# Kernel tuning notes

Hardware: AMD Instinct MI355X
Metric: run time of the kernel (lower is better)

## Reference

```python
import jax, jax.numpy as jnp
import numpy as np

C, H, R, INTER = 1024, 16, 16, 2816  # hidden, heads, lora rank, mlp intermediate
B, N = 2, 2048
EPS = 1e-5


def setup_inputs() -> dict:
    key = jax.random.key(0)
    ks = iter(jax.random.split(key, 48))
    w = lambda shape: jax.random.normal(next(ks), shape, jnp.float32) * 0.02
    d = {}
    d["x"] = jax.random.normal(next(ks), (B, N, C), jnp.float32)
    d["y"] = jax.random.normal(next(ks), (B, N, C), jnp.float32)
    d["c"] = jax.random.normal(next(ks), (B, C), jnp.float32)
    # LayerNorms
    d["gx_w"] = jnp.ones((C,)); d["gx_b"] = jnp.zeros((C,))
    d["gy_w"] = jnp.ones((C,)); d["gy_b"] = jnp.zeros((C,))
    # adaLN: SiLU -> Linear(C, 6C)
    d["ada_w"] = w((C, 6 * C)); d["ada_b"] = jnp.zeros((6 * C,))
    # two DoRA cross-attentions
    for p in ("xy", "yx"):
        d[p + "_qkv"] = w((C, 3 * C))
        d[p + "_mag"] = jnp.ones((1, H, 1, 1))
        d[p + "_la"] = w((C, R))
        d[p + "_lb"] = w((R, C))
        d[p + "_proj"] = w((C, C))
    # two HGRN recurrent attentions
    for p in ("ax", "ay"):
        d[p + "_wi"] = w((C, C))
        d[p + "_wf"] = w((C, C))
        d[p + "_wg"] = w((C, C))
        d[p + "_wo"] = w((C, C))
        d[p + "_gn"] = jnp.ones((C,))
    # two gated MLPs
    for p in ("mx", "my"):
        d[p + "_gate"] = w((C, 2 * INTER))
        d[p + "_down"] = w((INTER, C))
    return d


def _ln(v, wgt, b):
    m = v.mean(-1, keepdims=True)
    var = ((v - m) ** 2).mean(-1, keepdims=True)
    return (v - m) / jnp.sqrt(var + EPS) * wgt + b


def _modulate(v, shift, scale):
    return v * (1.0 + scale[:, None, :]) + shift[:, None, :]


def _dora_attn(q_in, Wqkv, mag, la, lb, Wp):
    # NOTE: source ignores key/value args -> self-attention on query stream
    Bq, Nq, Cq = q_in.shape
    D = Cq // H
    qkv = (q_in @ Wqkv).reshape(Bq, Nq, 3, H, D).transpose(2, 0, 3, 1, 4)
    q, k, v = qkv[0], qkv[1], qkv[2]  # [B,H,N,D]
    delta = (q_in @ la) @ lb  # LoRA delta injected into Q
    q = q + mag * delta.reshape(Bq, Nq, H, D).transpose(0, 2, 1, 3)
    attn = jax.nn.softmax(jnp.einsum('bhnd,bhmd->bhnm', q, k) * (D ** -0.5), axis=-1)
    o = jnp.einsum('bhnm,bhmd->bhnd', attn, v).transpose(0, 2, 1, 3).reshape(Bq, Nq, Cq)
    return o @ Wp


def _hgrn_attn(v, wi, wf, wg, wo, gn):
    Bv, Nv, Cv = v.shape
    D = Cv // H
    f = jax.nn.sigmoid(v @ wf)
    i = jax.nn.silu(v @ wi) * (1.0 - f)
    def step(h, ft_it):
        ft, it = ft_it
        h = ft * h + it
        return h, h
    _, hs = jax.lax.scan(step, jnp.zeros((Bv, Cv), v.dtype),
                         (f.transpose(1, 0, 2), i.transpose(1, 0, 2)))
    h = hs.transpose(1, 0, 2).reshape(Bv, Nv, H, D)
    h = h / jnp.sqrt((h * h).mean(-1, keepdims=True) + EPS)  # per-head RMSNorm
    h = (h * gn.reshape(H, D)).reshape(Bv, Nv, Cv)
    return (h * jax.nn.silu(v @ wg)) @ wo


def _mlp(v, wgate, wdown):
    u = v @ wgate
    gate, val = jnp.split(u, 2, axis=-1)
    return (jax.nn.silu(gate) * val) @ wdown


def reference(x, y, c, gx_w, gx_b, gy_w, gy_b, ada_w, ada_b,
              xy_qkv, xy_mag, xy_la, xy_lb, xy_proj,
              yx_qkv, yx_mag, yx_la, yx_lb, yx_proj,
              ax_wi, ax_wf, ax_wg, ax_wo, ax_gn,
              ay_wi, ay_wf, ay_wg, ay_wo, ay_gn,
              mx_gate, mx_down, my_gate, my_down):
    mods = jax.nn.silu(c) @ ada_w + ada_b
    sh_msa, sc_msa, g_msa, sh_mlp, sc_mlp, g_mlp = jnp.split(mods, 6, axis=1)
    x_norm = _ln(x, gx_w, gx_b)
    y_norm = _ln(y, gy_w, gy_b)
    x = x + g_msa[:, None, :] * _dora_attn(x_norm, xy_qkv, xy_mag, xy_la, xy_lb, xy_proj)
    y = y + g_msa[:, None, :] * _dora_attn(y_norm, yx_qkv, yx_mag, yx_la, yx_lb, yx_proj)
    x = x + g_msa[:, None, :] * _hgrn_attn(_modulate(x_norm, sh_msa, sc_msa), ax_wi, ax_wf, ax_wg, ax_wo, ax_gn)
    y = y + g_msa[:, None, :] * _hgrn_attn(_modulate(y_norm, sh_msa, sc_msa), ay_wi, ay_wf, ay_wg, ay_wo, ay_gn)
    x = x + g_mlp[:, None, :] * _mlp(_modulate(_ln(x, gx_w, gx_b), sh_mlp, sc_mlp), mx_gate, mx_down)
    y = y + g_mlp[:, None, :] * _mlp(_modulate(_ln(y, gy_w, gy_b), sh_mlp, sc_mlp), my_gate, my_down)
    return (x, y)
```

## Files before the change

kernel.cpp:

```cpp
#include <hip/hip_runtime.h>
#include <stdint.h>

#define NTOK 2048
#define CDIM 1024
#define ROWS 4096
#define MODS_STRIDE 6144
#define INTERDIM 2816
#define NCHUNK 32
#define CHLEN (NTOK/NCHUNK)

typedef unsigned short u16;
typedef __bf16 bf16x8 __attribute__((ext_vector_type(8)));
typedef float f32x4 __attribute__((ext_vector_type(4)));
typedef u16 u16x8 __attribute__((ext_vector_type(8)));

__device__ __forceinline__ float b2f(u16 u){
  union { unsigned int i; float f; } v; v.i = ((unsigned int)u) << 16; return v.f;
}
__device__ __forceinline__ u16 f2b(float f){
  union { float f; unsigned int i; } v; v.f = f;
  unsigned int i = v.i;
  unsigned int r = i + 0x7FFFu + ((i >> 16) & 1u);
  return (u16)(r >> 16);
}
__device__ __forceinline__ float sigm(float x){ return 1.f/(1.f+__expf(-x)); }
__device__ __forceinline__ float wredsum(float v){
#pragma unroll
  for (int o=32;o>0;o>>=1) v += __shfl_xor(v,o);
  return v;
}
__device__ __forceinline__ void async16(const void* g, void* l){
  __builtin_amdgcn_global_load_lds(
      (const __attribute__((address_space(1))) unsigned int*)g,
      (__attribute__((address_space(3))) unsigned int*)l, 16, 0, 0);
}

__global__ __launch_bounds__(512) void gemm_bt(
    const u16* __restrict__ Ain, const u16* __restrict__ Bt,
    int M, int N, int K, int epi,
    u16* __restrict__ outB,
    float* __restrict__ dest, const float* __restrict__ gate)
{
  __shared__ u16 smem[2][2][2][8192];

  const int nwg  = gridDim.x * gridDim.y;
  const int orig = blockIdx.y * gridDim.x + blockIdx.x;
  const int qch  = nwg >> 3, rch = nwg & 7;
  const int xcd  = orig & 7, loc = orig >> 3;
  const int swzb = (xcd < rch ? xcd*(qch+1) : rch*(qch+1) + (xcd-rch)*qch) + loc;
  const int m0 = (swzb / gridDim.x) * 256;
  const int n0 = (swzb % gridDim.x) * 256;

  const int kchunk = K / gridDim.z;
  const int kbase  = blockIdx.z * kchunk;
  const int NT = kchunk >> 6;

  const int tid = threadIdx.x;
  const int w = tid >> 6, lane = tid & 63;
  const int quad = lane >> 4, l16 = lane & 15;
  const int wm = w >> 2, wn = w & 3;
  const int sx = (l16 & 7) << 4;

  int soff[2];
#pragma unroll
  for (int j=0;j<2;++j){
    const int row = (w*2 + j)*8 + (lane >> 3);
    soff[j] = row*(K*2) + (((lane & 7) ^ (row & 7)) << 4);
  }

  const char* pA0 = (const char*)(Ain + (size_t)m0*K       + kbase);
  const char* pA1 = (const char*)(Ain + (size_t)(m0+128)*K + kbase);
  const char* pB0 = (const char*)(Bt  + (size_t)n0*K       + kbase);
  const char* pB1 = (const char*)(Bt  + (size_t)(n0+128)*K + kbase);

  auto stage = [&](const char* base, int t, u16* region){
#pragma unroll
    for (int j=0;j<2;++j)
      async16(base + (size_t)t*128 + soff[j], (char*)region + (w*2+j)*1024);
  };

  f32x4 acc[8][4] = {};
  bf16x8 af[4][2];
  bf16x8 bq[4][2];

  stage(pA0, 0, &smem[0][0][0][0]);
  stage(pA1, 0, &smem[0][0][1][0]);
  stage(pB0, 0, &smem[0][1][0][0]);
  stage(pB1, 0, &smem[0][1][1][0]);
  if (NT > 1){
    stage(pA0, 1, &smem[1][0][0][0]);
    asm volatile("s_waitcnt vmcnt(2)" ::: "memory");
  } else {
    asm volatile("s_waitcnt vmcnt(0)" ::: "memory");
  }
  __builtin_amdgcn_s_barrier();

#pragma unroll 1
  for (int t=0; t<NT; ++t){
    const int s  = t & 1;
    const int s1 = s ^ 1;
    const char* Ah = (const char*)&smem[s][0][wm][0];
    const char* Bh = (const char*)&smem[s][1][wn>>1][0];
    const int bb = (wn & 1) * 64;

#pragma unroll
    for (int mf=0; mf<4; ++mf)
#pragma unroll
      for (int ks=0; ks<2; ++ks){
        const int b = ((mf*16 + l16)*128 + ks*64 + quad*16) ^ sx;
        af[mf][ks] = *reinterpret_cast<const bf16x8*>(Ah + b);
      }
#pragma unroll
    for (int nf=0; nf<2; ++nf)
#pragma unroll
      for (int ks=0; ks<2; ++ks){
        const int b = ((bb + nf*16 + l16)*128 + ks*64 + quad*16) ^ sx;
        bq[nf][ks] = *reinterpret_cast<const bf16x8*>(Bh + b);
      }
    if (t+1 < NT) stage(pA1, t+1, &smem[s1][0][1][0]);
    __builtin_amdgcn_sched_barrier(0);
    __builtin_amdgcn_s_barrier();
    asm volatile("s_waitcnt lgkmcnt(0)" ::: "memory");
    __builtin_amdgcn_sched_barrier(0);
    __builtin_amdgcn_s_setprio(1);
#pragma unroll
    for (int mf=0; mf<4; ++mf)
#pragma unroll
      for (int nf=0; nf<2; ++nf)
#pragma unroll
        for (int ks=0; ks<2; ++ks)
          acc[mf][nf] = __builtin_amdgcn_mfma_f32_16x16x32_bf16(af[mf][ks], bq[nf][ks], acc[mf][nf], 0,0,0);
    __builtin_amdgcn_s_setprio(0);
    __builtin_amdgcn_sched_barrier(0);
    __builtin_amdgcn_s_barrier();

#pragma unroll
    for (int nf=0; nf<2; ++nf)
#pragma unroll
      for (int ks=0; ks<2; ++ks){
        const int b = ((bb + (2+nf)*16 + l16)*128 + ks*64 + quad*16) ^ sx;
        bq[2+nf][ks] = *reinterpret_cast<const bf16x8*>(Bh + b);
      }
    if (t+1 < NT) stage(pB0, t+1, &smem[s1][1][0][0]);
    __builtin_amdgcn_sched_barrier(0);
    __builtin_amdgcn_s_barrier();
    asm volatile("s_waitcnt lgkmcnt(0)" ::: "memory");
    __builtin_amdgcn_sched_barrier(0);
    __builtin_amdgcn_s_setprio(1);
#pragma unroll
    for (int mf=0; mf<4; ++mf)
#pragma unroll
      for (int nf=0; nf<2; ++nf)
#pragma unroll
        for (int ks=0; ks<2; ++ks)
          acc[mf][2+nf] = __builtin_amdgcn_mfma_f32_16x16x32_bf16(af[mf][ks], bq[2+nf][ks], acc[mf][2+nf], 0,0,0);
    __builtin_amdgcn_s_setprio(0);
    __builtin_amdgcn_sched_barrier(0);
    __builtin_amdgcn_s_barrier();

#pragma unroll
    for (int mf=0; mf<4; ++mf)
#pragma unroll
      for (int ks=0; ks<2; ++ks){
        const int b = ((64 + mf*16 + l16)*128 + ks*64 + quad*16) ^ sx;
        af[mf][ks] = *reinterpret_cast<const bf16x8*>(Ah + b);
      }
    if (t+1 < NT) stage(pB1, t+1, &smem[s1][1][1][0]);
    __builtin_amdgcn_sched_barrier(0);
    __builtin_amdgcn_s_barrier();
    asm volatile("s_waitcnt lgkmcnt(0)" ::: "memory");
    __builtin_amdgcn_sched_barrier(0);
    __builtin_amdgcn_s_setprio(1);
#pragma unroll
    for (int mf=0; mf<4; ++mf)
#pragma unroll
      for (int nf=0; nf<2; ++nf)
#pragma unroll
        for (int ks=0; ks<2; ++ks)
          acc[4+mf][2+nf] = __builtin_amdgcn_mfma_f32_16x16x32_bf16(af[mf][ks], bq[2+nf][ks], acc[4+mf][2+nf], 0,0,0);
    __builtin_amdgcn_s_setprio(0);
    __builtin_amdgcn_sched_barrier(0);
    __builtin_amdgcn_s_barrier();

    if (t+2 < NT) stage(pA0, t+2, &smem[s][0][0][0]);
    __builtin_amdgcn_sched_barrier(0);
    __builtin_amdgcn_s_barrier();
    __builtin_amdgcn_s_setprio(1);
#pragma unroll
    for (int mf=0; mf<4; ++mf)
#pragma unroll
      for (int nf=0; nf<2; ++nf)
#pragma unroll
        for (int ks=0; ks<2; ++ks)
          acc[4+mf][nf] = __builtin_amdgcn_mfma_f32_16x16x32_bf16(af[mf][ks], bq[nf][ks], acc[4+mf][nf], 0,0,0);
    __builtin_amdgcn_s_setprio(0);
    __builtin_amdgcn_sched_barrier(0);
    if (t+2 < NT) asm volatile("s_waitcnt vmcnt(2)" ::: "memory");
    else          asm volatile("s_waitcnt vmcnt(0)" ::: "memory");
    __builtin_amdgcn_s_barrier();
  }

#pragma unroll
  for (int i=0;i<8;++i){
    const int row = m0 + wm*128 + (i>>2)*64 + (i&3)*16 + quad*4;
#pragma unroll
    for (int j=0;j<4;++j){
      const int col = n0 + wn*64 + j*16 + l16;
#pragma unroll
      for (int r=0;r<4;++r){
        const float v = acc[i][j][r];
        const size_t idx = (size_t)(row + r)*N + col;
        if (epi==1){ outB[idx] = f2b(v); }
        else {
          const int b = (row + r) >> 11;
          atomicAdd(&dest[idx], gate[b*MODS_STRIDE + col] * v);
        }
      }
    }
  }
}

struct TDesc { const float* src; u16* dst; int rows; int cols; int base; int dstride; int doff; };
struct TPack { TDesc d[16]; };

__global__ __launch_bounds__(256) void transpose_all(TPack p, int nmat)
{
  __shared__ float t[32][33];
  const int bid = blockIdx.x;
  int mi = 0;
#pragma unroll 1
  while (mi+1 < nmat && bid >= p.d[mi+1].base) ++mi;
  const TDesc D = p.d[mi];
  const int tid2   = bid - D.base;
  const int tilesx = D.cols >> 5;
  const int r0 = (tid2 / tilesx) * 32;
  const int c0 = (tid2 % tilesx) * 32;
  const int tx = threadIdx.x & 31, ty = threadIdx.x >> 5;
  for (int i=ty;i<32;i+=8)
    t[i][tx] = D.src[(size_t)(r0+i)*D.cols + c0 + tx];
  __syncthreads();
  for (int i=ty;i<32;i+=8)
    D.dst[(size_t)(c0+i)*D.dstride + D.doff + r0 + tx] = f2b(t[tx][i]);
}

__global__ __launch_bounds__(256) void lora_fold(
    const float* __restrict__ la, const float* __restrict__ lb,
    const float* __restrict__ mag, u16* __restrict__ WqkvT)
{
  const unsigned idx = blockIdx.x*256u + threadIdx.x;
  const int k = idx & 1023, n = idx >> 10;
  float s = 0.f;
#pragma unroll
  for (int r=0;r<16;++r)
    s = fmaf(la[k*16+r], lb[r*1024+n], s);
  const float m = mag[n>>6];
  const unsigned o = (unsigned)n*1024u + k;
  WqkvT[o] = f2b(b2f(WqkvT[o]) + m*s);
}

__global__ __launch_bounds__(256) void ln_kernel(
    const float* __restrict__ xin,
    const float* __restrict__ w, const float* __restrict__ bias,
    const float* __restrict__ mods, int sh_off, int sc_off,
    u16* __restrict__ out_norm, u16* __restrict__ out_mod,
    float* __restrict__ out_xw)
{
  const int row = blockIdx.x;
  const int b = row >> 11;
  const int t = threadIdx.x;
  float v[4];
#pragma unroll
  for (int e=0;e<4;++e)
    v[e] = xin[(size_t)row*CDIM + t*4+e];
  float s  = v[0]+v[1]+v[2]+v[3];
  float ss = v[0]*v[0]+v[1]*v[1]+v[2]*v[2]+v[3]*v[3];
  s = wredsum(s); ss = wredsum(ss);
  __shared__ float rs[4], rss[4];
  const int wv = t>>6;
  if ((t&63)==0){ rs[wv]=s; rss[wv]=ss; }
  __syncthreads();
  s  = rs[0]+rs[1]+rs[2]+rs[3];
  ss = rss[0]+rss[1]+rss[2]+rss[3];
  const float mean = s * (1.f/1024.f);
  const float var  = ss * (1.f/1024.f) - mean*mean;
  const float rinv = rsqrtf(var + 1e-5f);
#pragma unroll
  for (int e=0;e<4;++e){
    const int c = t*4+e;
    const float nv = (v[e]-mean)*rinv*w[c] + bias[c];
    if (out_norm) out_norm[(size_t)row*CDIM+c] = f2b(nv);
    if (out_mod){
      const float sc = mods[b*MODS_STRIDE + sc_off + c];
      const float sh = mods[b*MODS_STRIDE + sh_off + c];
      out_mod[(size_t)row*CDIM+c] = f2b(nv*(1.f+sc)+sh);
    }
    if (out_xw) out_xw[(size_t)row*CDIM+c] = v[e];
  }
}

__global__ __launch_bounds__(256) void ada_init(
    const float* __restrict__ ab, float* __restrict__ mods)
{
  const int j = blockIdx.x*256 + threadIdx.x;
  const int jj = (j >= MODS_STRIDE) ? j - MODS_STRIDE : j;
  mods[j] = ab[jj];
}

__global__ __launch_bounds__(256) void ada_split(
    const float* __restrict__ cin, const float* __restrict__ aw,
    float* __restrict__ mods)
{
  const int j  = blockIdx.x*256 + threadIdx.x;
  const int k0 = blockIdx.y*64;
  float s0 = 0.f, s1 = 0.f;
  for (int k=k0; k<k0+64; ++k){
    const float wv = aw[(size_t)k*MODS_STRIDE + j];
    const float c0 = cin[k], c1 = cin[CDIM + k];
    s0 = fmaf(c0*sigm(c0), wv, s0);
    s1 = fmaf(c1*sigm(c1), wv, s1);
  }
  atomicAdd(&mods[j], s0);
  atomicAdd(&mods[MODS_STRIDE + j], s1);
}

__global__ __launch_bounds__(256) void attn_mfma(
    const u16* __restrict__ qkv, u16* __restrict__ AH)
{
  __shared__ u16 Kl[64*64];
  __shared__ u16 Vt[64*64];
  __shared__ u16 Pl[4][16*64];
  const int t = threadIdx.x;
  const int w = t>>6, lane = t&63;
  const int l16 = lane&15, quad = lane>>4;
  const int qt = blockIdx.x, h = blockIdx.y, b = blockIdx.z;
  const size_t rowbase = (size_t)b*NTOK;

  bf16x8 qf[2];
  {
    const size_t gr = rowbase + qt*64 + w*16 + l16;
    const u16* qp = qkv + gr*3072 + h*64;
#pragma unroll
    for (int kw=0; kw<2; ++kw){
      const u16x8 qa = *reinterpret_cast<const u16x8*>(qp + kw*32 + quad*8);
#pragma unroll
      for (int j=0;j<8;++j)
        qf[kw][j] = (__bf16)(b2f(qa[j]) * 0.125f);
    }
  }

  const u16* ksrc[2]; int kwr[2];
#pragma unroll
  for (int it=0; it<2; ++it){
    const int e = it*256 + t;
    const int key = e>>3, ch = e&7;
    ksrc[it] = qkv + (rowbase + key)*3072 + 1024 + h*64 + ch*8;
    kwr[it]  = key*128 + ((ch ^ (key&7)) << 4);
  }
  const u16* vsrc[2]; int vwr[2][8];
#pragma unroll
  for (int it=0; it<2; ++it){
    const int d0 = (w*2 + it)*8;
    vsrc[it] = qkv + (rowbase + lane)*3072 + 2048 + h*64 + d0;
#pragma unroll
    for (int j=0;j<8;++j){
      const int d = d0 + j;
      vwr[it][j] = d*128 + (((lane>>3) ^ (d&7)) << 4) + (lane&7)*2;
    }
  }
  int ra[4][2], pr[2], pw[4][2];
#pragma unroll
  for (int x=0; x<4; ++x)
#pragma unroll
    for (int kw=0; kw<2; ++kw)
      ra[x][kw] = (x*16 + l16)*128 + (((kw*4 + quad) ^ (l16&7)) << 4);
#pragma unroll
  for (int kw=0; kw<2; ++kw)
    pr[kw] = l16*128 + (((kw*4 + quad) ^ (l16&7)) << 4);
#pragma unroll
  for (int mt=0; mt<4; ++mt)
#pragma unroll
    for (int rp=0; rp<2; ++rp){
      const int bo = (mt*16 + quad*4 + rp*2)*2;
      pw[mt][rp] = l16*128 + (((bo>>4) ^ (l16&7)) << 4) + (bo & 15);
    }

  const size_t KSTRIDE = (size_t)64*3072;

  u16x8 kA[2], vA[2], kB[2], vB[2];
#pragma unroll
  for (int it=0; it<2; ++it){
    kA[it] = *reinterpret_cast<const u16x8*>(ksrc[it]);
    vA[it] = *reinterpret_cast<const u16x8*>(vsrc[it]);
  }

  float l_part = 0.f;
  f32x4 oacc[4] = {};
  char* const pb = (char*)&Pl[w][0];

  auto step = [&](u16x8 (&kk)[2], u16x8 (&vv)[2], int kbn,
                  u16x8 (&kn)[2], u16x8 (&vn)[2]){
#pragma unroll
    for (int it=0; it<2; ++it){
      *reinterpret_cast<u16x8*>((char*)Kl + kwr[it]) = kk[it];
#pragma unroll
      for (int j=0;j<8;++j)
        *reinterpret_cast<u16*>((char*)Vt + vwr[it][j]) = vv[it][j];
    }
    __syncthreads();
    {
      const size_t off = (size_t)kbn * KSTRIDE;
#pragma unroll
      for (int it=0; it<2; ++it){
        kn[it] = *reinterpret_cast<const u16x8*>(ksrc[it] + off);
        vn[it] = *reinterpret_cast<const u16x8*>(vsrc[it] + off);
      }
    }
    f32x4 sacc[4] = {};
#pragma unroll
    for (int kw=0; kw<2; ++kw)
#pragma unroll
      for (int mt=0; mt<4; ++mt){
        const bf16x8 af = *reinterpret_cast<const bf16x8*>((char*)Kl + ra[mt][kw]);
        sacc[mt] = __builtin_amdgcn_mfma_f32_16x16x32_bf16(af, qf[kw], sacc[mt], 0,0,0);
      }
#pragma unroll
    for (int mt=0; mt<4; ++mt)
#pragma unroll
      for (int r=0;r<4;++r){
        const float pv = __expf(sacc[mt][r]);
        sacc[mt][r] = pv;
        l_part += pv;
      }
#pragma unroll
    for (int mt=0; mt<4; ++mt)
#pragma unroll
      for (int rp=0; rp<2; ++rp){
        const unsigned hi = __float_as_uint(sacc[mt][rp*2+1]);
        const unsigned lo = __float_as_uint(sacc[mt][rp*2]);
        *reinterpret_cast<unsigned*>(pb + pw[mt][rp]) = (hi & 0xFFFF0000u) | (lo >> 16);
      }
#pragma unroll
    for (int kw=0; kw<2; ++kw){
      const bf16x8 pa = *reinterpret_cast<const bf16x8*>(pb + pr[kw]);
#pragma unroll
      for (int dt=0; dt<4; ++dt){
        const bf16x8 vb = *reinterpret_cast<const bf16x8*>((char*)Vt + ra[dt][kw]);
        oacc[dt] = __builtin_amdgcn_mfma_f32_16x16x32_bf16(pa, vb, oacc[dt], 0,0,0);
      }
    }
    __syncthreads();
  };

#pragma unroll 1
  for (int kb=0; kb<32; kb+=2){
    step(kA, vA, (kb+1 < 32 ? kb+1 : 31), kB, vB);
    step(kB, vB, (kb+2 < 32 ? kb+2 : 31), kA, vA);
  }

  float l_run = l_part;
  l_run += __shfl_xor(l_run, 16);
  l_run += __shfl_xor(l_run, 32);

  float li4[4];
#pragma unroll
  for (int r=0;r<4;++r) li4[r] = __shfl(l_run, quad*4+r);
#pragma unroll
  for (int r=0;r<4;++r){
    const size_t grow = rowbase + qt*64 + w*16 + quad*4 + r;
#pragma unroll
    for (int dt=0; dt<4; ++dt)
      AH[grow*2048 + h*64 + dt*16 + l16] = f2b(oacc[dt][r] / li4[r]);
  }
}

__global__ __launch_bounds__(256) void scan_p1(
    const u16* __restrict__ FIG, float* __restrict__ cA, float* __restrict__ cH)
{
  const unsigned int idx = blockIdx.x*256u + threadIdx.x;
  const unsigned int c = idx & 1023u, chunk = (idx>>10)&(NCHUNK-1), b = idx>>15;
  float A = 1.f, h = 0.f;
  const size_t base = ((size_t)b*NTOK + chunk*CHLEN) * 3072;
  for (int t=0;t<CHLEN;++t){
    const float F = b2f(FIG[base + (size_t)t*3072 + c]);
    const float I = b2f(FIG[base + (size_t)t*3072 + 1024 + c]);
    const float f = sigm(F);
    const float il = I*sigm(I) * (1.f - f);
    A *= f;
    h = fmaf(f, h, il);
  }
  cA[idx] = A; cH[idx] = h;
}

__global__ __launch_bounds__(256) void scan_p2(
    const float* __restrict__ cA, const float* __restrict__ cH, float* __restrict__ Hinit)
{
  const unsigned int idx = blockIdx.x*256u + threadIdx.x;
  const unsigned int b = idx>>10, c = idx&1023u;
  float h = 0.f;
#pragma unroll
  for (int ch=0;ch<NCHUNK;++ch){
    const unsigned int q = (b*NCHUNK + ch)*1024 + c;
    Hinit[q] = h;
    h = fmaf(cA[q], h, cH[q]);
  }
}

__global__ __launch_bounds__(256) void scan_p3(
    const u16* __restrict__ FIG, const float* __restrict__ Hinit, u16* __restrict__ Hb)
{
  const unsigned int idx = blockIdx.x*256u + threadIdx.x;
  const unsigned int c = idx & 1023u, chunk = (idx>>10)&(NCHUNK-1), b = idx>>15;
  float h = Hinit[idx];
  const size_t base = ((size_t)b*NTOK + chunk*CHLEN) * 3072;
  const size_t obase = ((size_t)b*NTOK + chunk*CHLEN) * CDIM;
  for (int t=0;t<CHLEN;++t){
    const float F = b2f(FIG[base + (size_t)t*3072 + c]);
    const float I = b2f(FIG[base + (size_t)t*3072 + 1024 + c]);
    const float f = sigm(F);
    const float il = I*sigm(I) * (1.f - f);
    h = fmaf(f, h, il);
    Hb[obase + (size_t)t*CDIM + c] = f2b(h);
  }
}

__global__ __launch_bounds__(256) void hgrn_post(
    const u16* __restrict__ Hb, const u16* __restrict__ FIG,
    const float* __restrict__ gn, u16* __restrict__ AH)
{
  const int row = blockIdx.x;
  const int t = threadIdx.x;
  float hv[4]; float ss = 0.f;
#pragma unroll
  for (int e=0;e<4;++e){
    hv[e] = b2f(Hb[(size_t)row*CDIM + t*4 + e]);
    ss = fmaf(hv[e], hv[e], ss);
  }
#pragma unroll
  for (int o=1;o<16;o<<=1) ss += __shfl_xor(ss, o);
  const float rinv = rsqrtf(ss*(1.f/64.f) + 1e-5f);
#pragma unroll
  for (int e=0;e<4;++e){
    const int c = t*4+e;
    const float g = b2f(FIG[(size_t)row*3072 + 2048 + c]);
    AH[(size_t)row*2048 + 1024 + c] = f2b(hv[e]*rinv*gn[c] * g*sigm(g));
  }
}

__global__ __launch_bounds__(256) void act_kernel(
    const u16* __restrict__ U, u16* __restrict__ A)
{
  const unsigned int i = blockIdx.x*256u + threadIdx.x;
  const unsigned int r = i / INTERDIM, j = i % INTERDIM;
  const float g = b2f(U[(size_t)r*(2*INTERDIM) + j]);
  const float v = b2f(U[(size_t)r*(2*INTERDIM) + INTERDIM + j]);
  A[i] = f2b(g*sigm(g)*v);
}

__global__ __launch_bounds__(256) void store_out(
    const float* __restrict__ xw, float* __restrict__ out)
{
  const unsigned int i = blockIdx.x*256u + threadIdx.x;
  out[i] = xw[i];
}

__global__ __launch_bounds__(256) void fill_fail(float* __restrict__ out)
{
  const unsigned int i = blockIdx.x*256u + threadIdx.x;
  out[i] = 1234.5f;
}

static void run_stream(hipStream_t stream,
    const float* Xin, const float* LNW, const float* LNB,
    const float* MAG, const float* LA, const float* LBw, const float* GN,
    float* mods, float* xw, float* outp,
    u16* WqkvT, const u16* WpwT, const u16* WhgrnT,
    const u16* WgateT, const u16* WdownT,
    u16* x_norm, u16* v_h, u16* qkvb, u16* delta, u16* AH,
    float* cA, float* cH, float* Hinit, u16* U, u16* actb)
{
  u16* FIG    = qkvb;
  u16* Hb     = delta;
  u16* mlp_in = x_norm;

  lora_fold<<<4096,256,0,stream>>>(LA, LBw, MAG, WqkvT);

  ln_kernel<<<ROWS,256,0,stream>>>(Xin, LNW, LNB, mods, 0, 1024, x_norm, v_h, xw);

  gemm_bt<<<dim3(12,16),512,0,stream>>>(x_norm, WqkvT, ROWS,3072,1024, 1, qkvb, nullptr, nullptr);
  attn_mfma<<<dim3(32,16,2),256,0,stream>>>(qkvb, AH);

  gemm_bt<<<dim3(12,16),512,0,stream>>>(v_h, WhgrnT, ROWS,3072,1024, 1, FIG, nullptr, nullptr);
  scan_p1<<<2*NCHUNK*1024/256,256,0,stream>>>(FIG, cA, cH);
  scan_p2<<<8,256,0,stream>>>(cA, cH, Hinit);
  scan_p3<<<2*NCHUNK*1024/256,256,0,stream>>>(FIG, Hinit, Hb);
  hgrn_post<<<ROWS,256,0,stream>>>(Hb, FIG, GN, AH);

  gemm_bt<<<dim3(4,16,4),512,0,stream>>>(AH, WpwT, ROWS,1024,2048, 2, nullptr, xw, mods+2048);

  ln_kernel<<<ROWS,256,0,stream>>>(xw, LNW, LNB, mods, 3072, 4096, nullptr, mlp_in, nullptr);
  gemm_bt<<<dim3(22,16),512,0,stream>>>(mlp_in, WgateT, ROWS,5632,1024, 1, U, nullptr, nullptr);
  act_kernel<<<ROWS*INTERDIM/256,256,0,stream>>>(U, actb);
  gemm_bt<<<dim3(4,16,4),512,0,stream>>>(actb, WdownT, ROWS,1024,2816, 2, nullptr, xw, mods+5120);

  store_out<<<ROWS*CDIM/256,256,0,stream>>>(xw, outp);
}

extern "C" void kernel_launch(void* const* d_in, const int* in_sizes, int n_in,
                              void* d_out, int out_size, void* d_ws, size_t ws_size,
                              hipStream_t stream)
{
  const float* X    = (const float*)d_in[0];
  const float* Y    = (const float*)d_in[1];
  const float* Cc   = (const float*)d_in[2];
  const float* GXW  = (const float*)d_in[3];
  const float* GXB  = (const float*)d_in[4];
  const float* GYW  = (const float*)d_in[5];
  const float* GYB  = (const float*)d_in[6];
  const float* ADAW = (const float*)d_in[7];
  const float* ADAB = (const float*)d_in[8];
  const float* XY_QKV = (const float*)d_in[9];
  const float* XY_MAG = (const float*)d_in[10];
  const float* XY_LA  = (const float*)d_in[11];
  const float* XY_LB  = (const float*)d_in[12];
  const float* XY_PROJ= (const float*)d_in[13];
  const float* YX_QKV = (const float*)d_in[14];
  const float* YX_MAG = (const float*)d_in[15];
  const float* YX_LA  = (const float*)d_in[16];
  const float* YX_LB  = (const float*)d_in[17];
  const float* YX_PROJ= (const float*)d_in[18];
  const float* AX_WI = (const float*)d_in[19];
  const float* AX_WF = (const float*)d_in[20];
  const float* AX_WG = (const float*)d_in[21];
  const float* AX_WO = (const float*)d_in[22];
  const float* AX_GN = (const float*)d_in[23];
  const float* AY_WI = (const float*)d_in[24];
  const float* AY_WF = (const float*)d_in[25];
  const float* AY_WG = (const float*)d_in[26];
  const float* AY_WO = (const float*)d_in[27];
  const float* AY_GN = (const float*)d_in[28];
  const float* MX_GATE = (const float*)d_in[29];
  const float* MX_DOWN = (const float*)d_in[30];
  const float* MY_GATE = (const float*)d_in[31];
  const float* MY_DOWN = (const float*)d_in[32];
  float* OUT = (float*)d_out;

  char* p = (char*)d_ws;
  size_t off = 0;
  auto alloc = [&](size_t bytes)->char*{
    char* r = p + off;
    off = (off + bytes + 255) & ~(size_t)255;
    return r;
  };
  float* mods  = (float*)alloc(2*MODS_STRIDE*sizeof(float));
  float* xw_x  = (float*)alloc((size_t)ROWS*CDIM*sizeof(float));
  float* xw_y  = (float*)alloc((size_t)ROWS*CDIM*sizeof(float));
  u16* WqkvT0  = (u16*)alloc((size_t)3072*1024*2);
  u16* WqkvT1  = (u16*)alloc((size_t)3072*1024*2);
  u16* WpwT0   = (u16*)alloc((size_t)1024*2048*2);
  u16* WpwT1   = (u16*)alloc((size_t)1024*2048*2);
  u16* WhgrnT0 = (u16*)alloc((size_t)3072*1024*2);
  u16* WhgrnT1 = (u16*)alloc((size_t)3072*1024*2);
  u16* WgateT0 = (u16*)alloc((size_t)5632*1024*2);
  u16* WgateT1 = (u16*)alloc((size_t)5632*1024*2);
  u16* WdownT0 = (u16*)alloc((size_t)1024*2816*2);
  u16* WdownT1 = (u16*)alloc((size_t)1024*2816*2);
  u16* x_norm  = (u16*)alloc((size_t)ROWS*CDIM*2);
  u16* v_h     = (u16*)alloc((size_t)ROWS*CDIM*2);
  u16* qkvb    = (u16*)alloc((size_t)ROWS*3072*2);
  u16* delta   = (u16*)alloc((size_t)ROWS*CDIM*2);
  u16* AH      = (u16*)alloc((size_t)ROWS*2048*2);
  float* cA    = (float*)alloc((size_t)2*NCHUNK*1024*sizeof(float));
  float* cH    = (float*)alloc((size_t)2*NCHUNK*1024*sizeof(float));
  float* Hinit = (float*)alloc((size_t)2*NCHUNK*1024*sizeof(float));
  u16* U       = (u16*)alloc((size_t)ROWS*5632*2);
  u16* actb    = (u16*)alloc((size_t)ROWS*INTERDIM*2);

  if (off > ws_size){
    fill_fail<<<(2*ROWS*CDIM)/256,256,0,stream>>>(OUT);
    return;
  }

  ada_init<<<2*MODS_STRIDE/256,256,0,stream>>>(ADAB, mods);
  ada_split<<<dim3(MODS_STRIDE/256,16),256,0,stream>>>(Cc, ADAW, mods);

  TPack tp; int base = 0; int ndesc = 0;
  auto add = [&](const float* s, u16* d2, int rows, int cols, int dstride, int doff){
    tp.d[ndesc].src = s; tp.d[ndesc].dst = d2;
    tp.d[ndesc].rows = rows; tp.d[ndesc].cols = cols; tp.d[ndesc].base = base;
    tp.d[ndesc].dstride = dstride; tp.d[ndesc].doff = doff;
    base += (rows>>5)*(cols>>5); ++ndesc;
  };
  add(XY_QKV,  WqkvT0, 1024, 3072, 1024, 0);
  add(XY_PROJ, WpwT0,  1024, 1024, 2048, 0);
  add(AX_WO,   WpwT0,  1024, 1024, 2048, 1024);
  add(AX_WF, WhgrnT0,               1024, 1024, 1024, 0);
  add(AX_WI, WhgrnT0 + 1024*1024,   1024, 1024, 1024, 0);
  add(AX_WG, WhgrnT0 + 2*1024*1024, 1024, 1024, 1024, 0);
  add(MX_GATE, WgateT0, 1024, 5632, 1024, 0);
  add(MX_DOWN, WdownT0, 2816, 1024, 2816, 0);
  add(YX_QKV,  WqkvT1, 1024, 3072, 1024, 0);
  add(YX_PROJ, WpwT1,  1024, 1024, 2048, 0);
  add(AY_WO,   WpwT1,  1024, 1024, 2048, 1024);
  add(AY_WF, WhgrnT1,               1024, 1024, 1024, 0);
  add(AY_WI, WhgrnT1 + 1024*1024,   1024, 1024, 1024, 0);
  add(AY_WG, WhgrnT1 + 2*1024*1024, 1024, 1024, 1024, 0);
  add(MY_GATE, WgateT1, 1024, 5632, 1024, 0);
  add(MY_DOWN, WdownT1, 2816, 1024, 2816, 0);
  transpose_all<<<base,256,0,stream>>>(tp, ndesc);

  run_stream(stream, X, GXW, GXB, XY_MAG, XY_LA, XY_LB, AX_GN,
             mods, xw_x, OUT,
             WqkvT0, WpwT0, WhgrnT0, WgateT0, WdownT0,
             x_norm, v_h, qkvb, delta, AH,
             cA, cH, Hinit, U, actb);

  run_stream(stream, Y, GYW, GYB, YX_MAG, YX_LA, YX_LB, AY_GN,
             mods, xw_y, OUT + (size_t)ROWS*CDIM,
             WqkvT1, WpwT1, WhgrnT1, WgateT1, WdownT1,
             x_norm, v_h, qkvb, delta, AH,
             cA, cH, Hinit, U, actb);
}
```

Before: 1.262 ms.

## Fuse SiLU-gating into gate GEMM epilogue and move attention to 32x32 MFMA

The MLP gate weight columns are interleaved during transpose so gate and value columns sit next to each other. The gate GEMM epilogue can then compute silu(g)*v with a lane shuffle and write the activation directly, which drops the separate act kernel and the U intermediate buffer. Separately, the attention kernel is rewritten to use 32x32x16 MFMAs over 128-query tiles. Probabilities are kept in registers through packed bf16 converts and permlane32 swaps instead of round-tripping through LDS. This adds register pressure and halves the attention grid size.

```diff
diff --git a/kernel.cpp b/kernel.cpp
--- a/kernel.cpp
+++ b/kernel.cpp
@@ -12,7 +12,9 @@
 typedef unsigned short u16;
 typedef __bf16 bf16x8 __attribute__((ext_vector_type(8)));
 typedef float f32x4 __attribute__((ext_vector_type(4)));
+typedef float f32x16 __attribute__((ext_vector_type(16)));
 typedef u16 u16x8 __attribute__((ext_vector_type(8)));
+typedef unsigned int u32x4 __attribute__((ext_vector_type(4)));
 
 __device__ __forceinline__ float b2f(u16 u){
   union { unsigned int i; float f; } v; v.i = ((unsigned int)u) << 16; return v.f;
@@ -33,6 +35,14 @@
   __builtin_amdgcn_global_load_lds(
       (const __attribute__((address_space(1))) unsigned int*)g,
       (__attribute__((address_space(3))) unsigned int*)l, 16, 0, 0);
+}
+__device__ __forceinline__ unsigned cvt_pk_bf16(float lo, float hi){
+  unsigned r;
+  asm("v_cvt_pk_bf16_f32 %0, %1, %2" : "=v"(r) : "v"(lo), "v"(hi));
+  return r;
+}
+__device__ __forceinline__ void permlane32_swap(unsigned &a, unsigned &b){
+  asm volatile("v_permlane32_swap_b32 %0, %1" : "+v"(a), "+v"(b));
 }
 
 __global__ __launch_bounds__(512) void gemm_bt(
@@ -211,7 +221,13 @@
         const float v = acc[i][j][r];
         const size_t idx = (size_t)(row + r)*N + col;
         if (epi==1){ outB[idx] = f2b(v); }
-        else {
+        else if (epi==3){
+          const float pv2 = __shfl_xor(v, 1);
+          if ((l16 & 1) == 0){
+            const float o = v*sigm(v)*pv2;
+            outB[(size_t)(row + r)*(N>>1) + (col>>1)] = f2b(o);
+          }
+        } else {
           const int b = (row + r) >> 11;
           atomicAdd(&dest[idx], gate[b*MODS_STRIDE + col] * v);
         }
@@ -220,7 +236,7 @@
   }
 }
 
-struct TDesc { const float* src; u16* dst; int rows; int cols; int base; int dstride; int doff; };
+struct TDesc { const float* src; u16* dst; int rows; int cols; int base; int dstride; int doff; int ileave; };
 struct TPack { TDesc d[16]; };
 
 __global__ __launch_bounds__(256) void transpose_all(TPack p, int nmat)
@@ -239,8 +255,11 @@
   for (int i=ty;i<32;i+=8)
     t[i][tx] = D.src[(size_t)(r0+i)*D.cols + c0 + tx];
   __syncthreads();
-  for (int i=ty;i<32;i+=8)
-    D.dst[(size_t)(c0+i)*D.dstride + D.doff + r0 + tx] = f2b(t[tx][i]);
+  for (int i=ty;i<32;i+=8){
+    int n = c0 + i;
+    if (D.ileave) n = (n < D.ileave) ? 2*n : 2*(n - D.ileave) + 1;
+    D.dst[(size_t)n*D.dstride + D.doff + r0 + tx] = f2b(t[tx][i]);
+  }
 }
 
 __global__ __launch_bounds__(256) void lora_fold(
@@ -328,23 +347,22 @@
 {
   __shared__ u16 Kl[64*64];
   __shared__ u16 Vt[64*64];
-  __shared__ u16 Pl[4][16*64];
   const int t = threadIdx.x;
   const int w = t>>6, lane = t&63;
-  const int l16 = lane&15, quad = lane>>4;
+  const int l32 = lane & 31, hi = lane >> 5;
   const int qt = blockIdx.x, h = blockIdx.y, b = blockIdx.z;
   const size_t rowbase = (size_t)b*NTOK;
 
-  bf16x8 qf[2];
+  bf16x8 qf[4];
   {
-    const size_t gr = rowbase + qt*64 + w*16 + l16;
+    const size_t gr = rowbase + qt*128 + w*32 + l32;
     const u16* qp = qkv + gr*3072 + h*64;
 #pragma unroll
-    for (int kw=0; kw<2; ++kw){
-      const u16x8 qa = *reinterpret_cast<const u16x8*>(qp + kw*32 + quad*8);
+    for (int ds=0; ds<4; ++ds){
+      const u16x8 qa = *reinterpret_cast<const u16x8*>(qp + ds*16 + hi*8);
 #pragma unroll
       for (int j=0;j<8;++j)
-        qf[kw][j] = (__bf16)(b2f(qa[j]) * 0.125f);
+        qf[ds][j] = (__bf16)(b2f(qa[j]) * 0.125f);
     }
   }
 
@@ -367,22 +385,24 @@
       vwr[it][j] = d*128 + (((lane>>3) ^ (d&7)) << 4) + (lane&7)*2;
     }
   }
-  int ra[4][2], pr[2], pw[4][2];
-#pragma unroll
-  for (int x=0; x<4; ++x)
-#pragma unroll
-    for (int kw=0; kw<2; ++kw)
-      ra[x][kw] = (x*16 + l16)*128 + (((kw*4 + quad) ^ (l16&7)) << 4);
-#pragma unroll
-  for (int kw=0; kw<2; ++kw)
-    pr[kw] = l16*128 + (((kw*4 + quad) ^ (l16&7)) << 4);
-#pragma unroll
-  for (int mt=0; mt<4; ++mt)
-#pragma unroll
-    for (int rp=0; rp<2; ++rp){
-      const int bo = (mt*16 + quad*4 + rp*2)*2;
-      pw[mt][rp] = l16*128 + (((bo>>4) ^ (l16&7)) << 4) + (bo & 15);
+  int kra[2][4];
+#pragma unroll
+  for (int st=0; st<2; ++st)
+#pragma unroll
+    for (int ds=0; ds<4; ++ds){
+      const int key = st*32 + l32;
+      kra[st][ds] = key*128 + (((ds*2 + hi) ^ (key&7)) << 4);
     }
+  int vra[2][2][2];
+#pragma unroll
+  for (int st=0; st<2; ++st)
+#pragma unroll
+    for (int ks=0; ks<2; ++ks)
+#pragma unroll
+      for (int dt=0; dt<2; ++dt){
+        const int d = dt*32 + l32;
+        vra[st][ks][dt] = d*128 + (((st*4 + ks*2 + hi) ^ (d&7)) << 4);
+      }
 
   const size_t KSTRIDE = (size_t)64*3072;
 
@@ -394,8 +414,7 @@
   }
 
   float l_part = 0.f;
-  f32x4 oacc[4] = {};
-  char* const pb = (char*)&Pl[w][0];
+  f32x16 oacc[2] = {};
 
   auto step = [&](u16x8 (&kk)[2], u16x8 (&vv)[2], int kbn,
                   u16x8 (&kn)[2], u16x8 (&vn)[2]){
@@ -415,37 +434,43 @@
         vn[it] = *reinterpret_cast<const u16x8*>(vsrc[it] + off);
       }
     }
-    f32x4 sacc[4] = {};
-#pragma unroll
-    for (int kw=0; kw<2; ++kw)
-#pragma unroll
-      for (int mt=0; mt<4; ++mt){
-        const bf16x8 af = *reinterpret_cast<const bf16x8*>((char*)Kl + ra[mt][kw]);
-        sacc[mt] = __builtin_amdgcn_mfma_f32_16x16x32_bf16(af, qf[kw], sacc[mt], 0,0,0);
-      }
-#pragma unroll
-    for (int mt=0; mt<4; ++mt)
-#pragma unroll
-      for (int r=0;r<4;++r){
-        const float pv = __expf(sacc[mt][r]);
-        sacc[mt][r] = pv;
+    f32x16 sacc[2] = {};
+#pragma unroll
+    for (int st=0; st<2; ++st)
+#pragma unroll
+      for (int ds=0; ds<4; ++ds){
+        const bf16x8 af = *reinterpret_cast<const bf16x8*>((char*)Kl + kra[st][ds]);
+        sacc[st] = __builtin_amdgcn_mfma_f32_32x32x16_bf16(af, qf[ds], sacc[st], 0,0,0);
+      }
+#pragma unroll
+    for (int st=0; st<2; ++st)
+#pragma unroll
+      for (int r=0;r<16;++r){
+        const float pv = __expf(sacc[st][r]);
+        sacc[st][r] = pv;
         l_part += pv;
       }
 #pragma unroll
-    for (int mt=0; mt<4; ++mt)
-#pragma unroll
-      for (int rp=0; rp<2; ++rp){
-        const unsigned hi = __float_as_uint(sacc[mt][rp*2+1]);
-        const unsigned lo = __float_as_uint(sacc[mt][rp*2]);
-        *reinterpret_cast<unsigned*>(pb + pw[mt][rp]) = (hi & 0xFFFF0000u) | (lo >> 16);
-      }
-#pragma unroll
-    for (int kw=0; kw<2; ++kw){
-      const bf16x8 pa = *reinterpret_cast<const bf16x8*>(pb + pr[kw]);
-#pragma unroll
-      for (int dt=0; dt<4; ++dt){
-        const bf16x8 vb = *reinterpret_cast<const bf16x8*>((char*)Vt + ra[dt][kw]);
-        oacc[dt] = __builtin_amdgcn_mfma_f32_16x16x32_bf16(pa, vb, oacc[dt], 0,0,0);
+    for (int st=0; st<2; ++st){
+      unsigned wd[8];
+#pragma unroll
+      for (int m=0;m<8;++m)
+        wd[m] = cvt_pk_bf16(sacc[st][2*m], sacc[st][2*m+1]);
+      permlane32_swap(wd[0], wd[2]);
+      permlane32_swap(wd[1], wd[3]);
+      permlane32_swap(wd[4], wd[6]);
+      permlane32_swap(wd[5], wd[7]);
+      u32x4 paw[2];
+      paw[0] = u32x4{wd[0], wd[1], wd[2], wd[3]};
+      paw[1] = u32x4{wd[4], wd[5], wd[6], wd[7]};
+#pragma unroll
+      for (int ks=0; ks<2; ++ks){
+        const bf16x8 pa = *reinterpret_cast<const bf16x8*>(&paw[ks]);
+#pragma unroll
+        for (int dt=0; dt<2; ++dt){
+          const bf16x8 vb = *reinterpret_cast<const bf16x8*>((char*)Vt + vra[st][ks][dt]);
+          oacc[dt] = __builtin_amdgcn_mfma_f32_32x32x16_bf16(pa, vb, oacc[dt], 0,0,0);
+        }
       }
     }
     __syncthreads();
@@ -457,19 +482,16 @@
     step(kB, vB, (kb+2 < 32 ? kb+2 : 31), kA, vA);
   }
 
-  float l_run = l_part;
-  l_run += __shfl_xor(l_run, 16);
-  l_run += __shfl_xor(l_run, 32);
-
-  float li4[4];
-#pragma unroll
-  for (int r=0;r<4;++r) li4[r] = __shfl(l_run, quad*4+r);
-#pragma unroll
-  for (int r=0;r<4;++r){
-    const size_t grow = rowbase + qt*64 + w*16 + quad*4 + r;
-#pragma unroll
-    for (int dt=0; dt<4; ++dt)
-      AH[grow*2048 + h*64 + dt*16 + l16] = f2b(oacc[dt][r] / li4[r]);
+  const float l_run = l_part + __shfl_xor(l_part, 32);
+
+#pragma unroll
+  for (int r=0;r<16;++r){
+    const int crow = (r&3) + 8*(r>>2) + 4*hi;
+    const float li = __shfl(l_run, crow);
+    const size_t grow = rowbase + qt*128 + w*32 + crow;
+#pragma unroll
+    for (int dt=0; dt<2; ++dt)
+      AH[grow*2048 + h*64 + dt*32 + l32] = f2b(oacc[dt][r] / li);
   }
 }
 
@@ -546,16 +568,6 @@
   }
 }
 
-__global__ __launch_bounds__(256) void act_kernel(
-    const u16* __restrict__ U, u16* __restrict__ A)
-{
-  const unsigned int i = blockIdx.x*256u + threadIdx.x;
-  const unsigned int r = i / INTERDIM, j = i % INTERDIM;
-  const float g = b2f(U[(size_t)r*(2*INTERDIM) + j]);
-  const float v = b2f(U[(size_t)r*(2*INTERDIM) + INTERDIM + j]);
-  A[i] = f2b(g*sigm(g)*v);
-}
-
 __global__ __launch_bounds__(256) void store_out(
     const float* __restrict__ xw, float* __restrict__ out)
 {
@@ -576,7 +588,7 @@
     u16* WqkvT, const u16* WpwT, const u16* WhgrnT,
     const u16* WgateT, const u16* WdownT,
     u16* x_norm, u16* v_h, u16* qkvb, u16* delta, u16* AH,
-    float* cA, float* cH, float* Hinit, u16* U, u16* actb)
+    float* cA, float* cH, float* Hinit, u16* actb)
 {
   u16* FIG    = qkvb;
   u16* Hb     = delta;
@@ -587,7 +599,7 @@
   ln_kernel<<<ROWS,256,0,stream>>>(Xin, LNW, LNB, mods, 0, 1024, x_norm, v_h, xw);
 
   gemm_bt<<<dim3(12,16),512,0,stream>>>(x_norm, WqkvT, ROWS,3072,1024, 1, qkvb, nullptr, nullptr);
-  attn_mfma<<<dim3(32,16,2),256,0,stream>>>(qkvb, AH);
+  attn_mfma<<<dim3(16,16,2),256,0,stream>>>(qkvb, AH);
 
   gemm_bt<<<dim3(12,16),512,0,stream>>>(v_h, WhgrnT, ROWS,3072,1024, 1, FIG, nullptr, nullptr);
   scan_p1<<<2*NCHUNK*1024/256,256,0,stream>>>(FIG, cA, cH);
@@ -598,8 +610,7 @@
   gemm_bt<<<dim3(4,16,4),512,0,stream>>>(AH, WpwT, ROWS,1024,2048, 2, nullptr, xw, mods+2048);
 
   ln_kernel<<<ROWS,256,0,stream>>>(xw, LNW, LNB, mods, 3072, 4096, nullptr, mlp_in, nullptr);
-  gemm_bt<<<dim3(22,16),512,0,stream>>>(mlp_in, WgateT, ROWS,5632,1024, 1, U, nullptr, nullptr);
-  act_kernel<<<ROWS*INTERDIM/256,256,0,stream>>>(U, actb);
+  gemm_bt<<<dim3(22,16),512,0,stream>>>(mlp_in, WgateT, ROWS,5632,1024, 3, actb, nullptr, nullptr);
   gemm_bt<<<dim3(4,16,4),512,0,stream>>>(actb, WdownT, ROWS,1024,2816, 2, nullptr, xw, mods+5120);
 
   store_out<<<ROWS*CDIM/256,256,0,stream>>>(xw, outp);
@@ -672,7 +683,6 @@
   float* cA    = (float*)alloc((size_t)2*NCHUNK*1024*sizeof(float));
   float* cH    = (float*)alloc((size_t)2*NCHUNK*1024*sizeof(float));
   float* Hinit = (float*)alloc((size_t)2*NCHUNK*1024*sizeof(float));
-  u16* U       = (u16*)alloc((size_t)ROWS*5632*2);
   u16* actb    = (u16*)alloc((size_t)ROWS*INTERDIM*2);
 
   if (off > ws_size){
@@ -684,39 +694,39 @@
   ada_split<<<dim3(MODS_STRIDE/256,16),256,0,stream>>>(Cc, ADAW, mods);
 
   TPack tp; int base = 0; int ndesc = 0;
-  auto add = [&](const float* s, u16* d2, int rows, int cols, int dstride, int doff){
+  auto add = [&](const float* s, u16* d2, int rows, int cols, int dstride, int doff, int il){
     tp.d[ndesc].src = s; tp.d[ndesc].dst = d2;
     tp.d[ndesc].rows = rows; tp.d[ndesc].cols = cols; tp.d[ndesc].base = base;
-    tp.d[ndesc].dstride = dstride; tp.d[ndesc].doff = doff;
+    tp.d[ndesc].dstride = dstride; tp.d[ndesc].doff = doff; tp.d[ndesc].ileave = il;
     base += (rows>>5)*(cols>>5); ++ndesc;
   };
-  add(XY_QKV,  WqkvT0, 1024, 3072, 1024, 0);
-  add(XY_PROJ, WpwT0,  1024, 1024, 2048, 0);
-  add(AX_WO,   WpwT0,  1024, 1024, 2048, 1024);
-  add(AX_WF, WhgrnT0,               1024, 1024, 1024, 0);
-  add(AX_WI, WhgrnT0 + 1024*1024,   1024, 1024, 1024, 0);
-  add(AX_WG, WhgrnT0 + 2*1024*1024, 1024, 1024, 1024, 0);
-  add(MX_GATE, WgateT0, 1024, 5632, 1024, 0);
-  add(MX_DOWN, WdownT0, 2816, 1024, 2816, 0);
-  add(YX_QKV,  WqkvT1, 1024, 3072, 1024, 0);
-  add(YX_PROJ, WpwT1,  1024, 1024, 2048, 0);
-  add(AY_WO,   WpwT1,  1024, 1024, 2048, 1024);
-  add(AY_WF, WhgrnT1,               1024, 1024, 1024, 0);
-  add(AY_WI, WhgrnT1 + 1024*1024,   1024, 1024, 1024, 0);
-  add(AY_WG, WhgrnT1 + 2*1024*1024, 1024, 1024, 1024, 0);
-  add(MY_GATE, WgateT1, 1024, 5632, 1024, 0);
-  add(MY_DOWN, WdownT1, 2816, 1024, 2816, 0);
+  add(XY_QKV,  WqkvT0, 1024, 3072, 1024, 0, 0);
+  add(XY_PROJ, WpwT0,  1024, 1024, 2048, 0, 0);
+  add(AX_WO,   WpwT0,  1024, 1024, 2048, 1024, 0);
+  add(AX_WF, WhgrnT0,               1024, 1024, 1024, 0, 0);
+  add(AX_WI, WhgrnT0 + 1024*1024,   1024, 1024, 1024, 0, 0);
+  add(AX_WG, WhgrnT0 + 2*1024*1024, 1024, 1024, 1024, 0, 0);
+  add(MX_GATE, WgateT0, 1024, 5632, 1024, 0, INTERDIM);
+  add(MX_DOWN, WdownT0, 2816, 1024, 2816, 0, 0);
+  add(YX_QKV,  WqkvT1, 1024, 3072, 1024, 0, 0);
+  add(YX_PROJ, WpwT1,  1024, 1024, 2048, 0, 0);
+  add(AY_WO,   WpwT1,  1024, 1024, 2048, 1024, 0);
+  add(AY_WF, WhgrnT1,               1024, 1024, 1024, 0, 0);
+  add(AY_WI, WhgrnT1 + 1024*1024,   1024, 1024, 1024, 0, 0);
+  add(AY_WG, WhgrnT1 + 2*1024*1024, 1024, 1024, 1024, 0, 0);
+  add(MY_GATE, WgateT1, 1024, 5632, 1024, 0, INTERDIM);
+  add(MY_DOWN, WdownT1, 2816, 1024, 2816, 0, 0);
   transpose_all<<<base,256,0,stream>>>(tp, ndesc);
 
   run_stream(stream, X, GXW, GXB, XY_MAG, XY_LA, XY_LB, AX_GN,
              mods, xw_x, OUT,
              WqkvT0, WpwT0, WhgrnT0, WgateT0, WdownT0,
              x_norm, v_h, qkvb, delta, AH,
-             cA, cH, Hinit, U, actb);
+             cA, cH, Hinit, actb);
 
   run_stream(stream, Y, GYW, GYB, YX_MAG, YX_LA, YX_LB, AY_GN,
              mods, xw_y, OUT + (size_t)ROWS*CDIM,
              WqkvT1, WpwT1, WhgrnT1, WgateT1, WdownT1,
              x_norm, v_h, qkvb, delta, AH,
-             cA, cH, Hinit, U, actb);
-}
+             cA, cH, Hinit, actb);
+}
```

New measurement: 1.277 ms. No clear change (+1.2%).
